# Optimization experiments

Measured on AMD Instinct MI355X. Metric: run time of the kernel, lower is better.

## Reference

```python
import jax, jax.numpy as jnp
import numpy as np

N, C, P, K = 100000, 64, 64, 16  # points, in_planes, planes, nsample
EPS = 1e-5

def _bn(y, g, b, m, v):
    # inference-mode batchnorm over channel (last) dim
    return (y - m) * (g * jax.lax.rsqrt(v + EPS)) + b

def setup_inputs() -> dict:
    key = jax.random.key(0)
    ks = jax.random.split(key, 12)
    p = jax.random.normal(ks[0], (N, 3), jnp.float32)
    x = jax.random.normal(ks[1], (N, C), jnp.float32)
    idx = jax.random.randint(ks[2], (N, K), 0, N, jnp.int32)
    s = 0.05
    w1 = jax.random.normal(ks[3], (C, P), jnp.float32) * s
    conv_w = jax.random.normal(ks[4], (P, P + 3), jnp.float32) * s  # Conv1d(P+3, P, 1) weight squeezed
    w3 = jax.random.normal(ks[5], (P, P), jnp.float32) * s
    def bn_params(k):
        k1, k2 = jax.random.split(k)
        return (jnp.ones((P,), jnp.float32),                      # gamma
                jnp.zeros((P,), jnp.float32),                     # beta
                jax.random.normal(k1, (P,), jnp.float32) * 0.01,  # running mean
                jnp.abs(jax.random.normal(k2, (P,), jnp.float32)) * 0.1 + 1.0)  # running var
    g1, b1, m1, v1 = bn_params(ks[6])
    g2, b2, m2, v2 = bn_params(ks[7])
    g3, b3, m3, v3 = bn_params(ks[8])
    return dict(p=p, x=x, idx=idx, w1=w1, g1=g1, b1=b1, m1=m1, v1=v1,
                conv_w=conv_w, g2=g2, b2=b2, m2=m2, v2=v2,
                w3=w3, g3=g3, b3=b3, m3=m3, v3=v3)

def reference(p, x, idx, w1, g1, b1, m1, v1, conv_w, g2, b2, m2, v2, w3, g3, b3, m3, v3):
    identity = x
    h = jax.nn.relu(_bn(x @ w1, g1, b1, m1, v1))                     # [N, P]
    # queryandgroup with use_xyz=True: concat(relative xyz, neighbor feats)
    rel = p[idx] - p[:, None, :]                                      # [N, K, 3]
    grouped = jnp.concatenate([rel, h[idx]], axis=-1)                 # [N, K, 3+P]
    e = jnp.einsum('nkc,oc->nko', grouped, conv_w)                    # conv1x1 -> [N, K, P]
    e = jax.nn.relu(_bn(e, g2, b2, m2, v2))
    f = jnp.max(e, axis=1)                                            # max over neighbors -> [N, P]
    out = jax.nn.relu(_bn(f @ w3, g3, b3, m3, v3) + identity)         # [N, P]
    return out
```

## Files before the change

kernel.cpp:

```cpp
#include <hip/hip_runtime.h>
#include <stdint.h>


#define EPS 1e-5f

typedef unsigned short u16;
typedef unsigned int u32;
typedef __attribute__((ext_vector_type(8))) short bf16x8;
typedef __attribute__((ext_vector_type(4))) float f32x4;

__device__ __forceinline__ float b2f(u16 u) { return __uint_as_float(((u32)u) << 16); }
__device__ __forceinline__ u16 f2b(float f) {
    u32 u = __float_as_uint(f);
    u32 r = u + 0x7fffu + ((u >> 16) & 1u);
    return (u16)(r >> 16);
}
__device__ __forceinline__ bool is_bf16(const void* g) { return ((const u32*)g)[0] == 0x3F803F80u; }
__device__ __forceinline__ float ldval(const void* p, size_t i, bool isbf) {
    return isbf ? b2f(((const u16*)p)[i]) : ((const float*)p)[i];
}
#define MFMA16(a, b, c) __builtin_amdgcn_mfma_f32_16x16x32_bf16(a, b, c, 0, 0, 0)

__device__ __forceinline__ bf16x8 asbf(uint4 u) {
    union { uint4 u; bf16x8 b; } c;
    c.u = u;
    return c.b;
}

__device__ __forceinline__ bf16x8 ldrow8(const void* base, size_t row, int coff, bool isbf) {
    if (isbf) {
        const u16* pp = (const u16*)base + row * 64 + coff;
        return asbf(*(const uint4*)pp);
    } else {
        const float* pp = (const float*)base + row * 64 + coff;
        float4 q0 = ((const float4*)pp)[0], q1 = ((const float4*)pp)[1];
        bf16x8 r;
        r[0] = (short)f2b(q0.x); r[1] = (short)f2b(q0.y);
        r[2] = (short)f2b(q0.z); r[3] = (short)f2b(q0.w);
        r[4] = (short)f2b(q1.x); r[5] = (short)f2b(q1.y);
        r[6] = (short)f2b(q1.z); r[7] = (short)f2b(q1.w);
        return r;
    }
}

__global__ void __launch_bounds__(256)
k_prep(const void* __restrict__ w1, const void* __restrict__ cw, const void* __restrict__ w3,
       const void* __restrict__ g1, const void* __restrict__ b1, const void* __restrict__ m1,
       const void* __restrict__ v1, const void* __restrict__ g2, const void* __restrict__ b2,
       const void* __restrict__ m2, const void* __restrict__ v2, const void* __restrict__ g3,
       const void* __restrict__ b3, const void* __restrict__ m3, const void* __restrict__ v3,
       uint4* __restrict__ w1f, uint4* __restrict__ cwf, uint4* __restrict__ w3f,
       float* __restrict__ bnst) {
    const bool isbf = is_bf16(g1);
    const int tid = blockIdx.x * blockDim.x + threadIdx.x;
    if (tid < 512) {
        int f = tid >> 6, lane = tid & 63;
        int ch = f >> 2, t = f & 3, quad = lane >> 4, c0 = lane & 15;
        union { uint4 u; bf16x8 b; } r;
#pragma unroll
        for (int j = 0; j < 8; ++j) {
            int c = ch * 32 + quad * 8 + j, o = t * 16 + c0;
            r.b[j] = (short)f2b(ldval(w1, (size_t)c * 64 + o, isbf));
        }
        w1f[f * 64 + lane] = r.u;
    } else if (tid < 1280) {
        int f = (tid - 512) >> 6, lane = tid & 63;
        int ch = f >> 2, t = f & 3, quad = lane >> 4, c0 = lane & 15;
        union { uint4 u; bf16x8 b; } r;
#pragma unroll
        for (int j = 0; j < 8; ++j) {
            int o = t * 16 + c0;
            short val;
            if (ch < 2) {
                int c = ch * 32 + quad * 8 + j;
                val = (short)f2b(ldval(cw, (size_t)o * 67 + 3 + c, isbf));
            } else {
                int pc = quad * 8 + j;
                val = (pc < 3) ? (short)f2b(ldval(cw, (size_t)o * 67 + pc, isbf)) : (short)0;
            }
            r.b[j] = val;
        }
        cwf[f * 64 + lane] = r.u;
    } else if (tid < 1792) {
        int f = (tid - 1280) >> 6, lane = tid & 63;
        int ch = f >> 2, t = f & 3, quad = lane >> 4, c0 = lane & 15;
        union { uint4 u; bf16x8 b; } r;
#pragma unroll
        for (int j = 0; j < 8; ++j) {
            int c = ch * 32 + quad * 8 + j, o = t * 16 + c0;
            r.b[j] = (short)f2b(ldval(w3, (size_t)c * 64 + o, isbf));
        }
        w3f[f * 64 + lane] = r.u;
    } else if (tid < 2176) {
        int id = tid - 1792;
        int bn = id >> 7, rem = id & 127, ch = rem & 63, which = rem >> 6;
        const void* g = (bn == 0) ? g1 : (bn == 1) ? g2 : g3;
        const void* b = (bn == 0) ? b1 : (bn == 1) ? b2 : b3;
        const void* m = (bn == 0) ? m1 : (bn == 1) ? m2 : m3;
        const void* v = (bn == 0) ? v1 : (bn == 1) ? v2 : v3;
        float gv = ldval(g, ch, isbf), bv = ldval(b, ch, isbf);
        float mv = ldval(m, ch, isbf), vv = ldval(v, ch, isbf);
        float s = gv * rsqrtf(vv + EPS);
        float t = bv - mv * s;
        bnst[bn * 128 + which * 64 + ch] = which ? t : s;
    }
}

__global__ void __launch_bounds__(256, 4)
k_h_mfma(const void* __restrict__ x, const void* __restrict__ p, const void* __restrict__ g1,
         const uint4* __restrict__ w1f, const float* __restrict__ bnst,
         float4* __restrict__ p4, u16* __restrict__ hbf, int N) {
    const bool isbf = is_bf16(g1);
    const int lane = threadIdx.x & 63, quad = lane >> 4, col = lane & 15;
    const int wave = blockIdx.x * (blockDim.x >> 6) + (threadIdx.x >> 6);
    const int nw = gridDim.x * (blockDim.x >> 6);
    bf16x8 B00 = asbf(w1f[0 * 64 + lane]), B01 = asbf(w1f[1 * 64 + lane]);
    bf16x8 B02 = asbf(w1f[2 * 64 + lane]), B03 = asbf(w1f[3 * 64 + lane]);
    bf16x8 B10 = asbf(w1f[4 * 64 + lane]), B11 = asbf(w1f[5 * 64 + lane]);
    bf16x8 B12 = asbf(w1f[6 * 64 + lane]), B13 = asbf(w1f[7 * 64 + lane]);
    f32x4 sv, tv;
#pragma unroll
    for (int t = 0; t < 4; ++t) {
        sv[t] = bnst[0 * 128 + 0 + t * 16 + col];
        tv[t] = bnst[0 * 128 + 64 + t * 16 + col];
    }
    const int nt = (N + 15) >> 4;
    for (int ti = wave; ti < nt; ti += nw) {
        const int n0 = ti * 16;
        int ra = n0 + col;
        if (ra > N - 1) ra = N - 1;
        bf16x8 A0 = ldrow8(x, (size_t)ra, quad * 8, isbf);
        bf16x8 A1 = ldrow8(x, (size_t)ra, 32 + quad * 8, isbf);
        if (p4 && quad == 0 && n0 + col < N) {
            int row = n0 + col;
            float4 pv;
            pv.x = ldval(p, (size_t)row * 3 + 0, isbf);
            pv.y = ldval(p, (size_t)row * 3 + 1, isbf);
            pv.z = ldval(p, (size_t)row * 3 + 2, isbf);
            pv.w = 0.f;
            p4[row] = pv;
        }
        f32x4 acc0 = {0.f, 0.f, 0.f, 0.f}, acc1 = acc0, acc2 = acc0, acc3 = acc0;
        acc0 = MFMA16(A0, B00, acc0); acc0 = MFMA16(A1, B10, acc0);
        acc1 = MFMA16(A0, B01, acc1); acc1 = MFMA16(A1, B11, acc1);
        acc2 = MFMA16(A0, B02, acc2); acc2 = MFMA16(A1, B12, acc2);
        acc3 = MFMA16(A0, B03, acc3); acc3 = MFMA16(A1, B13, acc3);
#define STT(acc, t)                                                            \
    {                                                                          \
        _Pragma("unroll") for (int r = 0; r < 4; ++r) {                        \
            int row = n0 + quad * 4 + r;                                       \
            if (row < N) {                                                     \
                float e = acc[r] * sv[t] + tv[t];                              \
                hbf[(size_t)row * 64 + (t)*16 + col] = f2b(fmaxf(e, 0.f));     \
            }                                                                  \
        }                                                                      \
    }
        STT(acc0, 0) STT(acc1, 1) STT(acc2, 2) STT(acc3, 3)
#undef STT
    }
}

__global__ void __launch_bounds__(256, 4)
k_w_mfma(u16* __restrict__ hw, u16* __restrict__ vbuf, const void* __restrict__ p,
         const void* __restrict__ g1, const uint4* __restrict__ cwf, int N) {
    const bool isbf = is_bf16(g1);
    const int lane = threadIdx.x & 63, quad = lane >> 4, col = lane & 15;
    const int wave = blockIdx.x * (blockDim.x >> 6) + (threadIdx.x >> 6);
    const int nw = gridDim.x * (blockDim.x >> 6);
    bf16x8 B00 = asbf(cwf[0 * 64 + lane]), B01 = asbf(cwf[1 * 64 + lane]);
    bf16x8 B02 = asbf(cwf[2 * 64 + lane]), B03 = asbf(cwf[3 * 64 + lane]);
    bf16x8 B10 = asbf(cwf[4 * 64 + lane]), B11 = asbf(cwf[5 * 64 + lane]);
    bf16x8 B12 = asbf(cwf[6 * 64 + lane]), B13 = asbf(cwf[7 * 64 + lane]);
    bf16x8 B20 = asbf(cwf[8 * 64 + lane]), B21 = asbf(cwf[9 * 64 + lane]);
    bf16x8 B22 = asbf(cwf[10 * 64 + lane]), B23 = asbf(cwf[11 * 64 + lane]);
    const int nt = (N + 15) >> 4;
    for (int ti = wave; ti < nt; ti += nw) {
        const int n0 = ti * 16;
        int ra = n0 + col;
        if (ra > N - 1) ra = N - 1;
        bf16x8 A0 = asbf(*(const uint4*)(hw + (size_t)ra * 64 + quad * 8));
        bf16x8 A1 = asbf(*(const uint4*)(hw + (size_t)ra * 64 + 32 + quad * 8));
        bf16x8 A2 = {0, 0, 0, 0, 0, 0, 0, 0};
        if (quad == 0) {
            A2[0] = (short)f2b(ldval(p, (size_t)ra * 3 + 0, isbf));
            A2[1] = (short)f2b(ldval(p, (size_t)ra * 3 + 1, isbf));
            A2[2] = (short)f2b(ldval(p, (size_t)ra * 3 + 2, isbf));
        }
        f32x4 z = {0.f, 0.f, 0.f, 0.f};
        f32x4 av0 = MFMA16(A2, B20, z), av1 = MFMA16(A2, B21, z);
        f32x4 av2 = MFMA16(A2, B22, z), av3 = MFMA16(A2, B23, z);
        f32x4 aw0 = MFMA16(A1, B10, MFMA16(A0, B00, av0));
        f32x4 aw1 = MFMA16(A1, B11, MFMA16(A0, B01, av1));
        f32x4 aw2 = MFMA16(A1, B12, MFMA16(A0, B02, av2));
        f32x4 aw3 = MFMA16(A1, B13, MFMA16(A0, B03, av3));
#define STW(accv, accw, t)                                                     \
    {                                                                          \
        _Pragma("unroll") for (int r = 0; r < 4; ++r) {                        \
            int row = n0 + quad * 4 + r;                                       \
            if (row < N) {                                                     \
                vbuf[(size_t)row * 64 + (t)*16 + col] = f2b(accv[r]);          \
                hw[(size_t)row * 64 + (t)*16 + col] = f2b(accw[r]);            \
            }                                                                  \
        }                                                                      \
    }
        STW(av0, aw0, 0) STW(av1, aw1, 1) STW(av2, aw2, 2) STW(av3, aw3, 3)
#undef STW
    }
}

__global__ void __launch_bounds__(256, 6)
k_gmax(const u16* __restrict__ wbuf, u16* __restrict__ vf, const int* __restrict__ idx,
       const float* __restrict__ bnst, int N) {
    const int lane = threadIdx.x & 63;
    const int wave = blockIdx.x * (blockDim.x >> 6) + (threadIdx.x >> 6);
    const int nw = gridDim.x * (blockDim.x >> 6);
    const float s2 = bnst[128 + lane];
    const float t2 = bnst[192 + lane];
    const int l31 = lane & 31;
    const int step = 2 * nw;
    int i = 2 * wave;
    if (i >= N) return;
    const size_t idxmax = (size_t)N * 16 - 1;
    size_t a0 = (size_t)i * 16 + l31;
    int jv = idx[a0 > idxmax ? idxmax : a0];
    for (; i < N; i += step) {
        size_t an = (size_t)(i + step) * 16 + l31;
        int jvn = idx[an > idxmax ? idxmax : an];
        const int ib = (i + 1 < N) ? i + 1 : i;
        u32 va = vf[(size_t)i * 64 + lane];
        u32 vb = vf[(size_t)ib * 64 + lane];
        u32 wa[16], wb[16];
#pragma unroll
        for (int k = 0; k < 16; ++k) {
            int ja = __builtin_amdgcn_readlane(jv, k);
            int jb = __builtin_amdgcn_readlane(jv, k + 16);
            wa[k] = wbuf[(size_t)ja * 64 + lane];
            wb[k] = wbuf[(size_t)jb * 64 + lane];
        }
        float mxa = b2f((u16)wa[0]), mna = mxa;
        float mxb = b2f((u16)wb[0]), mnb = mxb;
#pragma unroll
        for (int k = 1; k < 16; ++k) {
            float fa = b2f((u16)wa[k]);
            float fb = b2f((u16)wb[k]);
            mxa = fmaxf(mxa, fa); mna = fminf(mna, fa);
            mxb = fmaxf(mxb, fb); mnb = fminf(mnb, fb);
        }
        float ca = t2 - s2 * b2f((u16)va);
        float cb = t2 - s2 * b2f((u16)vb);
        float fa = fmaxf(fmaxf(s2 * mxa, s2 * mna) + ca, 0.f);
        float fb = fmaxf(fmaxf(s2 * mxb, s2 * mnb) + cb, 0.f);
        vf[(size_t)i * 64 + lane] = f2b(fa);
        if (i + 1 < N) vf[(size_t)(i + 1) * 64 + lane] = f2b(fb);
        jv = jvn;
    }
}

template <bool FORCE_BF16>
__global__ void __launch_bounds__(256, 4)
k_conv_mfma(const u16* __restrict__ hbf, const float4* __restrict__ p4,
            const int* __restrict__ idx, const uint4* __restrict__ cwf,
            const float* __restrict__ bnst, const void* __restrict__ g2,
            void* __restrict__ fout, int N) {
    const bool isbf = is_bf16(g2);
    const int lane = threadIdx.x & 63, quad = lane >> 4, col = lane & 15;
    const int wave = blockIdx.x * (blockDim.x >> 6) + (threadIdx.x >> 6);
    const int nw = gridDim.x * (blockDim.x >> 6);
    bf16x8 B00 = asbf(cwf[0 * 64 + lane]), B01 = asbf(cwf[1 * 64 + lane]);
    bf16x8 B02 = asbf(cwf[2 * 64 + lane]), B03 = asbf(cwf[3 * 64 + lane]);
    bf16x8 B10 = asbf(cwf[4 * 64 + lane]), B11 = asbf(cwf[5 * 64 + lane]);
    bf16x8 B12 = asbf(cwf[6 * 64 + lane]), B13 = asbf(cwf[7 * 64 + lane]);
    bf16x8 B20 = asbf(cwf[8 * 64 + lane]), B21 = asbf(cwf[9 * 64 + lane]);
    bf16x8 B22 = asbf(cwf[10 * 64 + lane]), B23 = asbf(cwf[11 * 64 + lane]);
    f32x4 sv, tv;
#pragma unroll
    for (int t = 0; t < 4; ++t) {
        sv[t] = bnst[1 * 128 + 0 + t * 16 + col];
        tv[t] = bnst[1 * 128 + 64 + t * 16 + col];
    }
    int i = wave;
    if (i >= N) return;
    const int step = nw;
    int i1 = i + step;
    int i1c = (i1 < N) ? i1 : N - 1;
    int j0 = idx[(size_t)i * 16 + col];
    int j1 = idx[(size_t)i1c * 16 + col];
    const uint4* r0 = (const uint4*)(hbf + (size_t)j0 * 64);
    uint4 h0_c = r0[quad], h1_c = r0[4 + quad];
    float4 pj_c = p4[j0];
    float4 pn_c = p4[i];
    for (; i < N; i += step, i1 += step) {
        const int i2 = i1 + step;
        const int i2c = (i2 < N) ? i2 : N - 1;
        int j2 = idx[(size_t)i2c * 16 + col];
        const uint4* rn = (const uint4*)(hbf + (size_t)j1 * 64);
        uint4 h0_n = rn[quad], h1_n = rn[4 + quad];
        const int i1cc = (i1 < N) ? i1 : N - 1;
        float4 pj_n = p4[j1];
        float4 pn_n = p4[i1cc];
        bf16x8 A2 = {0, 0, 0, 0, 0, 0, 0, 0};
        if (quad == 0) {
            A2[0] = (short)f2b(pj_c.x - pn_c.x);
            A2[1] = (short)f2b(pj_c.y - pn_c.y);
            A2[2] = (short)f2b(pj_c.z - pn_c.z);
        }
        f32x4 z = {0.f, 0.f, 0.f, 0.f};
        f32x4 acc0 = z, acc1 = z, acc2 = z, acc3 = z;
        bf16x8 a0 = asbf(h0_c), a1 = asbf(h1_c);
        acc0 = MFMA16(a0, B00, acc0);
        acc1 = MFMA16(a0, B01, acc1);
        acc2 = MFMA16(a0, B02, acc2);
        acc3 = MFMA16(a0, B03, acc3);
        acc0 = MFMA16(a1, B10, acc0);
        acc1 = MFMA16(a1, B11, acc1);
        acc2 = MFMA16(a1, B12, acc2);
        acc3 = MFMA16(a1, B13, acc3);
        acc0 = MFMA16(A2, B20, acc0);
        acc1 = MFMA16(A2, B21, acc1);
        acc2 = MFMA16(A2, B22, acc2);
        acc3 = MFMA16(A2, B23, acc3);
#define RED(acc, t, dst)                                                       \
    {                                                                          \
        float mx = fmaxf(fmaxf(acc[0], acc[1]), fmaxf(acc[2], acc[3]));        \
        float mn = fminf(fminf(acc[0], acc[1]), fminf(acc[2], acc[3]));        \
        mx = fmaxf(mx, __shfl_xor(mx, 16));                                    \
        mn = fminf(mn, __shfl_xor(mn, 16));                                    \
        mx = fmaxf(mx, __shfl_xor(mx, 32));                                    \
        mn = fminf(mn, __shfl_xor(mn, 32));                                    \
        float e = fmaxf(sv[t] * mx + tv[t], sv[t] * mn + tv[t]);               \
        dst = fmaxf(e, 0.f);                                                   \
    }
        float f0, f1, f2, f3;
        RED(acc0, 0, f0) RED(acc1, 1, f1) RED(acc2, 2, f2) RED(acc3, 3, f3)
#undef RED
        float fv = (lane < 16) ? f0 : (lane < 32) ? f1 : (lane < 48) ? f2 : f3;
        if (FORCE_BF16 || isbf)
            ((u16*)fout)[(size_t)i * 64 + lane] = f2b(fv);
        else
            ((float*)fout)[(size_t)i * 64 + lane] = fv;
        j0 = j1; j1 = j2;
        h0_c = h0_n; h1_c = h1_n;
        pj_c = pj_n; pn_c = pn_n;
    }
}

template <bool FIN_BF16_ALWAYS>
__global__ void __launch_bounds__(256, 4)
k_out_mfma(const void* __restrict__ fin, const void* __restrict__ x,
           const uint4* __restrict__ w3f, const float* __restrict__ bnst,
           const void* __restrict__ g3, void* __restrict__ out, int N) {
    const bool isbf = is_bf16(g3);
    const bool finbf = FIN_BF16_ALWAYS ? true : isbf;
    const int lane = threadIdx.x & 63, quad = lane >> 4, col = lane & 15;
    const int wave = blockIdx.x * (blockDim.x >> 6) + (threadIdx.x >> 6);
    const int nw = gridDim.x * (blockDim.x >> 6);
    bf16x8 B00 = asbf(w3f[0 * 64 + lane]), B01 = asbf(w3f[1 * 64 + lane]);
    bf16x8 B02 = asbf(w3f[2 * 64 + lane]), B03 = asbf(w3f[3 * 64 + lane]);
    bf16x8 B10 = asbf(w3f[4 * 64 + lane]), B11 = asbf(w3f[5 * 64 + lane]);
    bf16x8 B12 = asbf(w3f[6 * 64 + lane]), B13 = asbf(w3f[7 * 64 + lane]);
    f32x4 sv, tv;
#pragma unroll
    for (int t = 0; t < 4; ++t) {
        sv[t] = bnst[2 * 128 + 0 + t * 16 + col];
        tv[t] = bnst[2 * 128 + 64 + t * 16 + col];
    }
    const int nt = (N + 15) >> 4;
    for (int ti = wave; ti < nt; ti += nw) {
        const int n0 = ti * 16;
        int ra = n0 + col;
        if (ra > N - 1) ra = N - 1;
        bf16x8 A0 = ldrow8(fin, (size_t)ra, quad * 8, finbf);
        bf16x8 A1 = ldrow8(fin, (size_t)ra, 32 + quad * 8, finbf);
        f32x4 acc0 = {0.f, 0.f, 0.f, 0.f}, acc1 = acc0, acc2 = acc0, acc3 = acc0;
        acc0 = MFMA16(A0, B00, acc0); acc0 = MFMA16(A1, B10, acc0);
        acc1 = MFMA16(A0, B01, acc1); acc1 = MFMA16(A1, B11, acc1);
        acc2 = MFMA16(A0, B02, acc2); acc2 = MFMA16(A1, B12, acc2);
        acc3 = MFMA16(A0, B03, acc3); acc3 = MFMA16(A1, B13, acc3);
#define STT(acc, t)                                                            \
    {                                                                          \
        _Pragma("unroll") for (int r = 0; r < 4; ++r) {                        \
            int row = n0 + quad * 4 + r;                                       \
            if (row < N) {                                                     \
                int o_ = (t)*16 + col;                                         \
                float e = acc[r] * sv[t] + tv[t] +                             \
                          ldval(x, (size_t)row * 64 + o_, isbf);               \
                e = fmaxf(e, 0.f);                                             \
                if (isbf)                                                      \
                    ((u16*)out)[(size_t)row * 64 + o_] = f2b(e);               \
                else                                                           \
                    ((float*)out)[(size_t)row * 64 + o_] = e;                  \
            }                                                                  \
        }                                                                      \
    }
        STT(acc0, 0) STT(acc1, 1) STT(acc2, 2) STT(acc3, 3)
#undef STT
    }
}

__device__ __forceinline__ void load_col64(const void* w, int lane, bool isbf, float* col) {
#pragma unroll
    for (int c = 0; c < 64; ++c) col[c] = ldval(w, (size_t)c * 64 + lane, isbf);
}
__device__ __forceinline__ float dot64(const void* x, size_t off, bool isbf, const float* col) {
    float a0 = 0.f;
#pragma unroll
    for (int c = 0; c < 64; ++c) a0 += ldval(x, off + c, isbf) * col[c];
    return a0;
}
__device__ __forceinline__ void bn_st(const void* g, const void* b, const void* m,
                                      const void* v, int o, bool isbf, float& s, float& t) {
    float gv = ldval(g, o, isbf), bv = ldval(b, o, isbf);
    float mv = ldval(m, o, isbf), vv = ldval(v, o, isbf);
    s = gv * rsqrtf(vv + EPS);
    t = bv - mv * s;
}
__global__ void __launch_bounds__(256) k_mono(const void* __restrict__ p, const void* __restrict__ x,
                                              const int* __restrict__ idx, const void* __restrict__ w1,
                                              const void* __restrict__ g1, const void* __restrict__ b1,
                                              const void* __restrict__ m1, const void* __restrict__ v1,
                                              const void* __restrict__ cw, const void* __restrict__ g2,
                                              const void* __restrict__ b2, const void* __restrict__ m2,
                                              const void* __restrict__ v2, const void* __restrict__ w3,
                                              const void* __restrict__ g3, const void* __restrict__ b3,
                                              const void* __restrict__ m3, const void* __restrict__ v3,
                                              void* __restrict__ out, int N) {
    const bool isbf = is_bf16(g1);
    const int lane = threadIdx.x & 63;
    const int wave = blockIdx.x * (blockDim.x >> 6) + (threadIdx.x >> 6);
    const int nw = gridDim.x * (blockDim.x >> 6);
    float w1col[64];
    load_col64(w1, lane, isbf, w1col);
    float w3col[64];
    load_col64(w3, lane, isbf, w3col);
    float s1, t1, s2, t2, s3, t3;
    bn_st(g1, b1, m1, v1, lane, isbf, s1, t1);
    bn_st(g2, b2, m2, v2, lane, isbf, s2, t2);
    bn_st(g3, b3, m3, v3, lane, isbf, s3, t3);
    for (int n = wave; n < N; n += nw) {
        const int4* ir = (const int4*)(idx + (size_t)n * 16);
        float pnx = ldval(p, (size_t)n * 3 + 0, isbf);
        float pny = ldval(p, (size_t)n * 3 + 1, isbf);
        float pnz = ldval(p, (size_t)n * 3 + 2, isbf);
        float fmx = 0.f;
        for (int kk = 0; kk < 4; ++kk) {
            const int4 iv = ir[kk];
#pragma unroll
            for (int t = 0; t < 4; ++t) {
                const int j = (t == 0) ? iv.x : (t == 1) ? iv.y : (t == 2) ? iv.z : iv.w;
                float hr = dot64(x, (size_t)j * 64, isbf, w1col);
                float hv = fmaxf(hr * s1 + t1, 0.f);
                float a0 = (ldval(p, (size_t)j * 3 + 0, isbf) - pnx) * ldval(cw, (size_t)lane * 67 + 0, isbf) +
                           (ldval(p, (size_t)j * 3 + 1, isbf) - pny) * ldval(cw, (size_t)lane * 67 + 1, isbf) +
                           (ldval(p, (size_t)j * 3 + 2, isbf) - pnz) * ldval(cw, (size_t)lane * 67 + 2, isbf);
#pragma unroll
                for (int c = 0; c < 64; ++c)
                    a0 += __shfl(hv, c) * ldval(cw, (size_t)lane * 67 + 3 + c, isbf);
                fmx = fmaxf(fmx, a0 * s2 + t2);
            }
        }
        float a = 0.f;
#pragma unroll
        for (int c = 0; c < 64; ++c) a += __shfl(fmx, c) * w3col[c];
        float r = a * s3 + t3 + ldval(x, (size_t)n * 64 + lane, isbf);
        r = fmaxf(r, 0.f);
        if (isbf)
            ((u16*)out)[(size_t)n * 64 + lane] = f2b(r);
        else
            ((float*)out)[(size_t)n * 64 + lane] = r;
    }
}

extern "C" void kernel_launch(void* const* d_in, const int* in_sizes, int n_in,
                              void* d_out, int out_size, void* d_ws, size_t ws_size,
                              hipStream_t stream) {
    const void* p = d_in[0];
    const void* x = d_in[1];
    const int* idx = (const int*)d_in[2];
    const void* w1 = d_in[3];
    const void* g1 = d_in[4];
    const void* b1 = d_in[5];
    const void* m1 = d_in[6];
    const void* v1 = d_in[7];
    const void* cw = d_in[8];
    const void* g2 = d_in[9];
    const void* b2 = d_in[10];
    const void* m2 = d_in[11];
    const void* v2 = d_in[12];
    const void* w3 = d_in[13];
    const void* g3 = d_in[14];
    const void* b3 = d_in[15];
    const void* m3 = d_in[16];
    const void* v3 = d_in[17];
    const int N = in_sizes[0] / 3;

    const int blk = 256;
    const int nt = (N + 15) >> 4;
    const int gh = (nt + 3) >> 2;
    const int gg = 2048;

    const size_t hb = (size_t)N * 64 * sizeof(u16);
    const size_t p4b = (size_t)N * sizeof(float4);
    const size_t packb = 8192 + 12288 + 8192 + 1536;
    const size_t need_big = 256 + 2 * hb + packb;
    const size_t need_h = 256 + hb + p4b + packb;

    if (ws_size >= need_big) {
        char* base = (char*)d_ws + 256;
        u16* b1buf = (u16*)base;
        u16* b2buf = (u16*)(base + hb);
        char* rest = base + 2 * hb;
        uint4* w1f = (uint4*)rest;
        uint4* cwf = (uint4*)(rest + 8192);
        uint4* w3f = (uint4*)(rest + 8192 + 12288);
        float* bnst = (float*)(rest + 8192 + 12288 + 8192);
        k_prep<<<9, blk, 0, stream>>>(w1, cw, w3, g1, b1, m1, v1, g2, b2, m2, v2,
                                      g3, b3, m3, v3, w1f, cwf, w3f, bnst);
        k_h_mfma<<<gh, blk, 0, stream>>>(x, p, g1, w1f, bnst, nullptr, b1buf, N);
        k_w_mfma<<<gh, blk, 0, stream>>>(b1buf, b2buf, p, g1, cwf, N);
        k_gmax<<<gg, blk, 0, stream>>>(b1buf, b2buf, idx, bnst, N);
        k_out_mfma<true><<<gh, blk, 0, stream>>>((const void*)b2buf, x, w3f, bnst, g3,
                                                 d_out, N);
    } else if (ws_size >= need_h) {
        char* base = (char*)d_ws + 256;
        u16* h = (u16*)base;
        char* rest = base + hb;
        float4* p4 = (float4*)rest;
        uint4* w1f = (uint4*)(rest + p4b);
        uint4* cwf = (uint4*)(rest + p4b + 8192);
        uint4* w3f = (uint4*)(rest + p4b + 8192 + 12288);
        float* bnst = (float*)(rest + p4b + 8192 + 12288 + 8192);
        k_prep<<<9, blk, 0, stream>>>(w1, cw, w3, g1, b1, m1, v1, g2, b2, m2, v2,
                                      g3, b3, m3, v3, w1f, cwf, w3f, bnst);
        k_h_mfma<<<gh, blk, 0, stream>>>(x, p, g1, w1f, bnst, p4, h, N);
        k_conv_mfma<false><<<2048, blk, 0, stream>>>(h, p4, idx, cwf, bnst, g2, d_out, N);
        k_out_mfma<false><<<gh, blk, 0, stream>>>((const void*)d_out, x, w3f, bnst, g3,
                                                  d_out, N);
    } else {
        k_mono<<<2048, blk, 0, stream>>>(p, x, idx, w1, g1, b1, m1, v1, cw, g2, b2, m2, v2,
                                         w3, g3, b3, m3, v3, d_out, N);
    }
}
```

Before: 173.2 us.

## Quantize gathered neighbor features to per-channel 8-bit before the max gather

k_w_mfma now also tracks per-channel min and max of the neighbor term. It reduces them through shuffles, shared memory and global atomics into order-preserving integer keys. A new k_q kernel quantizes that buffer to uint8 per channel, and a new k_gmax8 gathers the 1-byte codes, takes max/min over the 16 neighbors, dequantizes and applies the BN/ReLU. The goal is to halve the bytes moved by the random neighbor gather. The cost is an extra quantization pass, atomics, one point per wave instead of two, and reduced precision in the gathered features.

```diff
diff --git a/kernel.cpp b/kernel.cpp
--- a/kernel.cpp
+++ b/kernel.cpp
@@ -6,6 +6,7 @@
 
 typedef unsigned short u16;
 typedef unsigned int u32;
+typedef unsigned char u8;
 typedef __attribute__((ext_vector_type(8))) short bf16x8;
 typedef __attribute__((ext_vector_type(4))) float f32x4;
 
@@ -14,6 +15,14 @@
     u32 u = __float_as_uint(f);
     u32 r = u + 0x7fffu + ((u >> 16) & 1u);
     return (u16)(r >> 16);
+}
+__device__ __forceinline__ u32 fkey(float f) {
+    u32 i = __float_as_uint(f);
+    return (i & 0x80000000u) ? ~i : (i | 0x80000000u);
+}
+__device__ __forceinline__ float fdec(u32 k) {
+    u32 i = (k & 0x80000000u) ? (k & 0x7FFFFFFFu) : ~k;
+    return __uint_as_float(i);
 }
 __device__ __forceinline__ bool is_bf16(const void* g) { return ((const u32*)g)[0] == 0x3F803F80u; }
 __device__ __forceinline__ float ldval(const void* p, size_t i, bool isbf) {
@@ -50,7 +59,7 @@
        const void* __restrict__ m2, const void* __restrict__ v2, const void* __restrict__ g3,
        const void* __restrict__ b3, const void* __restrict__ m3, const void* __restrict__ v3,
        uint4* __restrict__ w1f, uint4* __restrict__ cwf, uint4* __restrict__ w3f,
-       float* __restrict__ bnst) {
+       float* __restrict__ bnst, u32* __restrict__ rkeys) {
     const bool isbf = is_bf16(g1);
     const int tid = blockIdx.x * blockDim.x + threadIdx.x;
     if (tid < 512) {
@@ -103,6 +112,9 @@
         float s = gv * rsqrtf(vv + EPS);
         float t = bv - mv * s;
         bnst[bn * 128 + which * 64 + ch] = which ? t : s;
+    } else if (tid < 2304) {
+        int id = tid - 2176;
+        rkeys[id] = (id < 64) ? 0u : 0xFFFFFFFFu;
     }
 }
 
@@ -162,7 +174,8 @@
 
 __global__ void __launch_bounds__(256, 4)
 k_w_mfma(u16* __restrict__ hw, u16* __restrict__ vbuf, const void* __restrict__ p,
-         const void* __restrict__ g1, const uint4* __restrict__ cwf, int N) {
+         const void* __restrict__ g1, const uint4* __restrict__ cwf,
+         u32* __restrict__ rkeys, int N) {
     const bool isbf = is_bf16(g1);
     const int lane = threadIdx.x & 63, quad = lane >> 4, col = lane & 15;
     const int wave = blockIdx.x * (blockDim.x >> 6) + (threadIdx.x >> 6);
@@ -173,6 +186,9 @@
     bf16x8 B12 = asbf(cwf[6 * 64 + lane]), B13 = asbf(cwf[7 * 64 + lane]);
     bf16x8 B20 = asbf(cwf[8 * 64 + lane]), B21 = asbf(cwf[9 * 64 + lane]);
     bf16x8 B22 = asbf(cwf[10 * 64 + lane]), B23 = asbf(cwf[11 * 64 + lane]);
+    float wmx[4], wmn[4];
+#pragma unroll
+    for (int t = 0; t < 4; ++t) { wmx[t] = -3.4e38f; wmn[t] = 3.4e38f; }
     const int nt = (N + 15) >> 4;
     for (int ti = wave; ti < nt; ti += nw) {
         const int n0 = ti * 16;
@@ -199,60 +215,108 @@
             int row = n0 + quad * 4 + r;                                       \
             if (row < N) {                                                     \
                 vbuf[(size_t)row * 64 + (t)*16 + col] = f2b(accv[r]);          \
-                hw[(size_t)row * 64 + (t)*16 + col] = f2b(accw[r]);            \
+                u16 rw = f2b(accw[r]);                                         \
+                hw[(size_t)row * 64 + (t)*16 + col] = rw;                      \
+                float wrv = b2f(rw);                                           \
+                wmx[t] = fmaxf(wmx[t], wrv);                                   \
+                wmn[t] = fminf(wmn[t], wrv);                                   \
             }                                                                  \
         }                                                                      \
     }
         STW(av0, aw0, 0) STW(av1, aw1, 1) STW(av2, aw2, 2) STW(av3, aw3, 3)
 #undef STW
     }
-}
-
-__global__ void __launch_bounds__(256, 6)
-k_gmax(const u16* __restrict__ wbuf, u16* __restrict__ vf, const int* __restrict__ idx,
-       const float* __restrict__ bnst, int N) {
+#pragma unroll
+    for (int t = 0; t < 4; ++t) {
+        wmx[t] = fmaxf(wmx[t], __shfl_xor(wmx[t], 16));
+        wmx[t] = fmaxf(wmx[t], __shfl_xor(wmx[t], 32));
+        wmn[t] = fminf(wmn[t], __shfl_xor(wmn[t], 16));
+        wmn[t] = fminf(wmn[t], __shfl_xor(wmn[t], 32));
+    }
+    __shared__ float smx[4][64], smn[4][64];
+    const int wv = threadIdx.x >> 6;
+    if (quad == 0) {
+#pragma unroll
+        for (int t = 0; t < 4; ++t) {
+            smx[wv][t * 16 + col] = wmx[t];
+            smn[wv][t * 16 + col] = wmn[t];
+        }
+    }
+    __syncthreads();
+    if (threadIdx.x < 64) {
+        int ch = threadIdx.x;
+        float m1 = fmaxf(fmaxf(smx[0][ch], smx[1][ch]), fmaxf(smx[2][ch], smx[3][ch]));
+        float m2 = fminf(fminf(smn[0][ch], smn[1][ch]), fminf(smn[2][ch], smn[3][ch]));
+        atomicMax(&rkeys[ch], fkey(m1));
+        atomicMin(&rkeys[64 + ch], fkey(m2));
+    }
+}
+
+__global__ void __launch_bounds__(256)
+k_q(const u16* __restrict__ w, u8* __restrict__ wq, const u32* __restrict__ rkeys, int N) {
+    __shared__ float smn[64], sinv[64];
+    if (threadIdx.x < 64) {
+        float mx = fdec(rkeys[threadIdx.x]);
+        float mn = fdec(rkeys[64 + threadIdx.x]);
+        smn[threadIdx.x] = mn;
+        sinv[threadIdx.x] = (mx > mn) ? 255.f / (mx - mn) : 0.f;
+    }
+    __syncthreads();
+    int tid = blockIdx.x * 256 + threadIdx.x;
+    if (tid >= N * 8) return;
+    int c0 = (tid & 7) * 8;
+    uint4 wv = ((const uint4*)w)[tid];
+    u32 out0 = 0, out1 = 0;
+#pragma unroll
+    for (int j = 0; j < 8; ++j) {
+        u32 word = (j < 2) ? wv.x : (j < 4) ? wv.y : (j < 6) ? wv.z : wv.w;
+        u16 hw = (j & 1) ? (u16)(word >> 16) : (u16)(word & 0xFFFFu);
+        float val = b2f(hw);
+        int ch = c0 + j;
+        int q = (int)roundf((val - smn[ch]) * sinv[ch]);
+        q = (q < 0) ? 0 : (q > 255 ? 255 : q);
+        if (j < 4) out0 |= ((u32)q) << (8 * j);
+        else       out1 |= ((u32)q) << (8 * (j - 4));
+    }
+    uint2 o; o.x = out0; o.y = out1;
+    ((uint2*)wq)[tid] = o;
+}
+
+__global__ void __launch_bounds__(256, 8)
+k_gmax8(const u8* __restrict__ wq, u16* __restrict__ vf, const int* __restrict__ idx,
+        const float* __restrict__ bnst, const u32* __restrict__ rkeys, int N) {
     const int lane = threadIdx.x & 63;
     const int wave = blockIdx.x * (blockDim.x >> 6) + (threadIdx.x >> 6);
     const int nw = gridDim.x * (blockDim.x >> 6);
+    float mx = fdec(rkeys[lane]);
+    float mn = fdec(rkeys[64 + lane]);
+    float sc = (mx - mn) * (1.f / 255.f);
     const float s2 = bnst[128 + lane];
     const float t2 = bnst[192 + lane];
-    const int l31 = lane & 31;
-    const int step = 2 * nw;
-    int i = 2 * wave;
+    const float a = s2 * sc;
+    const float c0 = s2 * mn + t2;
+    int i = wave;
     if (i >= N) return;
-    const size_t idxmax = (size_t)N * 16 - 1;
-    size_t a0 = (size_t)i * 16 + l31;
-    int jv = idx[a0 > idxmax ? idxmax : a0];
-    for (; i < N; i += step) {
-        size_t an = (size_t)(i + step) * 16 + l31;
-        int jvn = idx[an > idxmax ? idxmax : an];
-        const int ib = (i + 1 < N) ? i + 1 : i;
-        u32 va = vf[(size_t)i * 64 + lane];
-        u32 vb = vf[(size_t)ib * 64 + lane];
-        u32 wa[16], wb[16];
+    int jv = idx[(size_t)i * 16 + (lane & 15)];
+    for (; i < N; i += nw) {
+        const int inx = i + nw;
+        int jn = idx[(size_t)((inx < N) ? inx : i) * 16 + (lane & 15)];
+        u32 q[16];
 #pragma unroll
         for (int k = 0; k < 16; ++k) {
-            int ja = __builtin_amdgcn_readlane(jv, k);
-            int jb = __builtin_amdgcn_readlane(jv, k + 16);
-            wa[k] = wbuf[(size_t)ja * 64 + lane];
-            wb[k] = wbuf[(size_t)jb * 64 + lane];
-        }
-        float mxa = b2f((u16)wa[0]), mna = mxa;
-        float mxb = b2f((u16)wb[0]), mnb = mxb;
+            int j = __builtin_amdgcn_readlane(jv, k);
+            q[k] = wq[(size_t)j * 64 + lane];
+        }
+        u32 vraw = vf[(size_t)i * 64 + lane];
+        u32 qmx = q[0], qmn = q[0];
 #pragma unroll
         for (int k = 1; k < 16; ++k) {
-            float fa = b2f((u16)wa[k]);
-            float fb = b2f((u16)wb[k]);
-            mxa = fmaxf(mxa, fa); mna = fminf(mna, fa);
-            mxb = fmaxf(mxb, fb); mnb = fminf(mnb, fb);
-        }
-        float ca = t2 - s2 * b2f((u16)va);
-        float cb = t2 - s2 * b2f((u16)vb);
-        float fa = fmaxf(fmaxf(s2 * mxa, s2 * mna) + ca, 0.f);
-        float fb = fmaxf(fmaxf(s2 * mxb, s2 * mnb) + cb, 0.f);
-        vf[(size_t)i * 64 + lane] = f2b(fa);
-        if (i + 1 < N) vf[(size_t)(i + 1) * 64 + lane] = f2b(fb);
-        jv = jvn;
+            qmx = (q[k] > qmx) ? q[k] : qmx;
+            qmn = (q[k] < qmn) ? q[k] : qmn;
+        }
+        float e = fmaxf(a * (float)qmx, a * (float)qmn) + c0 - s2 * b2f((u16)vraw);
+        vf[(size_t)i * 64 + lane] = f2b(fmaxf(e, 0.f));
+        jv = jn;
     }
 }
 
@@ -497,27 +561,31 @@
     const int nt = (N + 15) >> 4;
     const int gh = (nt + 3) >> 2;
     const int gg = 2048;
+    const int gq = (N * 8 + blk - 1) / blk;
 
     const size_t hb = (size_t)N * 64 * sizeof(u16);
     const size_t p4b = (size_t)N * sizeof(float4);
     const size_t packb = 8192 + 12288 + 8192 + 1536;
-    const size_t need_big = 256 + 2 * hb + packb;
+    const size_t need_r10 = 256 + 2 * hb + hb / 2 + packb + 512;
     const size_t need_h = 256 + hb + p4b + packb;
 
-    if (ws_size >= need_big) {
+    if (ws_size >= need_r10) {
         char* base = (char*)d_ws + 256;
         u16* b1buf = (u16*)base;
         u16* b2buf = (u16*)(base + hb);
-        char* rest = base + 2 * hb;
+        u8* wq = (u8*)(base + 2 * hb);
+        char* rest = base + 2 * hb + hb / 2;
         uint4* w1f = (uint4*)rest;
         uint4* cwf = (uint4*)(rest + 8192);
         uint4* w3f = (uint4*)(rest + 8192 + 12288);
         float* bnst = (float*)(rest + 8192 + 12288 + 8192);
+        u32* rkeys = (u32*)(rest + packb);
         k_prep<<<9, blk, 0, stream>>>(w1, cw, w3, g1, b1, m1, v1, g2, b2, m2, v2,
-                                      g3, b3, m3, v3, w1f, cwf, w3f, bnst);
+                                      g3, b3, m3, v3, w1f, cwf, w3f, bnst, rkeys);
         k_h_mfma<<<gh, blk, 0, stream>>>(x, p, g1, w1f, bnst, nullptr, b1buf, N);
-        k_w_mfma<<<gh, blk, 0, stream>>>(b1buf, b2buf, p, g1, cwf, N);
-        k_gmax<<<gg, blk, 0, stream>>>(b1buf, b2buf, idx, bnst, N);
+        k_w_mfma<<<gh, blk, 0, stream>>>(b1buf, b2buf, p, g1, cwf, rkeys, N);
+        k_q<<<gq, blk, 0, stream>>>(b1buf, wq, rkeys, N);
+        k_gmax8<<<gg, blk, 0, stream>>>(wq, b2buf, idx, bnst, rkeys, N);
         k_out_mfma<true><<<gh, blk, 0, stream>>>((const void*)b2buf, x, w3f, bnst, g3,
                                                  d_out, N);
     } else if (ws_size >= need_h) {
@@ -529,8 +597,9 @@
         uint4* cwf = (uint4*)(rest + p4b + 8192);
         uint4* w3f = (uint4*)(rest + p4b + 8192 + 12288);
         float* bnst = (float*)(rest + p4b + 8192 + 12288 + 8192);
+        u32* rkeys = (u32*)(rest + p4b + packb);
         k_prep<<<9, blk, 0, stream>>>(w1, cw, w3, g1, b1, m1, v1, g2, b2, m2, v2,
-                                      g3, b3, m3, v3, w1f, cwf, w3f, bnst);
+                                      g3, b3, m3, v3, w1f, cwf, w3f, bnst, rkeys);
         k_h_mfma<<<gh, blk, 0, stream>>>(x, p, g1, w1f, bnst, p4, h, N);
         k_conv_mfma<false><<<2048, blk, 0, stream>>>(h, p4, idx, cwf, bnst, g2, d_out, N);
         k_out_mfma<false><<<gh, blk, 0, stream>>>((const void*)d_out, x, w3f, bnst, g3,
```

Result: slower. 196.6 us (+13.5%).
